# Kernel tuning notes

Measured on AMD Instinct MI355X. Metric: run time of the kernel, lower is better.

## Reference

```python
import jax, jax.numpy as jnp
import numpy as np

DIM = 256      # in_channels == hidden_channels
INNER = 256    # heads * dim_head
HEADS = 4
DH = 64        # dim_head = hidden_channels // num_heads
EDGE_DIM = 512 # 2 * in_channels
FF = 1024      # 4 * dim ff expansion
DEPTH = 2
OUT = 1
N = 50000      # two stacked graphs of 25000 nodes
E = 100000
HALF = 25000


def setup_inputs() -> dict:
    key = jax.random.key(0)
    ks = iter(jax.random.split(key, 32))

    def lin(fan_in, fan_out):
        w = jax.random.normal(next(ks), (DEPTH, fan_in, fan_out), jnp.float32) * (1.0 / np.sqrt(fan_in))
        b = jnp.zeros((DEPTH, fan_out), jnp.float32)
        return w, b

    x = jax.random.normal(next(ks), (N, DIM), jnp.float32)
    edge_index = jax.random.randint(next(ks), (2, E), 0, HALF, dtype=jnp.int32)
    Wq, bq = lin(DIM, INNER)
    Wkv, bkv = lin(DIM, 2 * INNER)
    We, be = lin(EDGE_DIM, INNER)
    Wo, bo = lin(INNER, DIM)
    W1, b1 = lin(DIM, FF)
    W2, b2 = lin(FF, DIM)
    g_attn = jax.random.normal(next(ks), (DEPTH, 3 * DIM, 1), jnp.float32) * (1.0 / np.sqrt(3 * DIM))
    g_ff = jax.random.normal(next(ks), (DEPTH, 3 * DIM, 1), jnp.float32) * (1.0 / np.sqrt(3 * DIM))
    ln1_g = jnp.ones((DEPTH, DIM), jnp.float32); ln1_b = jnp.zeros((DEPTH, DIM), jnp.float32)
    ln2_g = jnp.ones((DEPTH, DIM), jnp.float32); ln2_b = jnp.zeros((DEPTH, DIM), jnp.float32)
    Wout = jax.random.normal(next(ks), (DIM, OUT), jnp.float32) * (1.0 / np.sqrt(DIM))
    bout = jnp.zeros((OUT,), jnp.float32)
    return dict(x=x, edge_index=edge_index, ln1_g=ln1_g, ln1_b=ln1_b, Wq=Wq, bq=bq,
                Wkv=Wkv, bkv=bkv, We=We, be=be, Wo=Wo, bo=bo, g_attn=g_attn,
                ln2_g=ln2_g, ln2_b=ln2_b, W1=W1, b1=b1, W2=W2, b2=b2, g_ff=g_ff,
                Wout=Wout, bout=bout)


def _layer_norm(x, g, b):
    mu = jnp.mean(x, axis=-1, keepdims=True)
    var = jnp.mean(jnp.square(x - mu), axis=-1, keepdims=True)
    return (x - mu) * jax.lax.rsqrt(var + 1e-5) * g + b


def _gated_residual(x, res, w):
    # gate = sigmoid(Linear_no_bias(cat(x, res, x - res)))
    gate = jax.nn.sigmoid(jnp.concatenate([x, res, x - res], axis=-1) @ w)  # [n,1]
    return x * gate + res * (1.0 - gate)


def _forward(x, edge_index, ln1_g, ln1_b, Wq, bq, Wkv, bkv, We, be, Wo, bo, g_attn,
             ln2_g, ln2_b, W1, b1, W2, b2, g_ff, Wout, bout):
    src, dst = edge_index[0], edge_index[1]
    # edge_attr = cat(x[src], x[dst]) as built in DeepGraphTransformer_mse.forward
    edge_attr = jnp.concatenate([x[src], x[dst]], axis=-1)  # [E, 2*DIM]
    nodes = x
    n = nodes.shape[0]
    scale = DH ** -0.5
    for l in range(DEPTH):
        xn = _layer_norm(nodes, ln1_g[l], ln1_b[l])
        q = xn @ Wq[l] + bq[l]                                   # [n, INNER]
        k, v = jnp.split(xn @ Wkv[l] + bkv[l], 2, axis=-1)       # [n, INNER] each
        e = edge_attr @ We[l] + be[l]                            # [E, INNER]
        qe = q[dst].reshape(-1, HEADS, DH)                       # [E,H,Dh]
        ke = (k[src] + e).reshape(-1, HEADS, DH)
        ve = (v[src] + e).reshape(-1, HEADS, DH)
        sim = jnp.einsum('ehd,ehd->eh', qe, ke) * scale          # [E,H]
        smax = jax.ops.segment_max(sim, dst, num_segments=n)     # [n,H] (-inf for empty)
        ez = jnp.exp(sim - smax[dst])
        denom = jax.ops.segment_sum(ez, dst, num_segments=n)
        attn = ez / denom[dst]                                   # softmax over incoming edges
        agg = jax.ops.segment_sum(attn[:, :, None] * ve, dst, num_segments=n)
        attn_out = agg.reshape(n, INNER) @ Wo[l] + bo[l]         # [n, DIM]
        nodes = _gated_residual(attn_out, nodes, g_attn[l])
        xn2 = _layer_norm(nodes, ln2_g[l], ln2_b[l])
        h = jax.nn.gelu(xn2 @ W1[l] + b1[l], approximate=False) @ W2[l] + b2[l]
        nodes = _gated_residual(h, nodes, g_ff[l])
    z = nodes @ Wout + bout                                      # [n, OUT]
    return z


def reference(x, edge_index, ln1_g, ln1_b, Wq, bq, Wkv, bkv, We, be, Wo, bo, g_attn,
              ln2_g, ln2_b, W1, b1, W2, b2, g_ff, Wout, bout):
    z = _forward(x, edge_index, ln1_g, ln1_b, Wq, bq, Wkv, bkv, We, be, Wo, bo, g_attn,
                 ln2_g, ln2_b, W1, b1, W2, b2, g_ff, Wout, bout)
    half = z.shape[0] // 2
    z_old, z_new = z[:half], z[half:]
    return (z_new.reshape(-1), z_old, z_new)
```

## Files before the change

kernel.cpp:

```cpp
#include <hip/hip_runtime.h>
#include <cmath>

#define N_NODES 50000
#define N_EDGES 100000
#define HALF_N  25000
#define DIM     256
#define NDEPTH  2
#define MAXDEG  64

#define WT_QKVE 0
#define WT_WO   393216
#define WT_W1   524288
#define WT_W2   786432
#define WT_LAYER 1048576

typedef __bf16 bf16;
typedef bf16 bf16x8 __attribute__((ext_vector_type(8)));
typedef bf16 bf16x4 __attribute__((ext_vector_type(4)));
typedef float f32x4 __attribute__((ext_vector_type(4)));

__device__ __forceinline__ void lds_barrier() {
  asm volatile("s_waitcnt lgkmcnt(0)" ::: "memory");
  __builtin_amdgcn_s_barrier();
  __builtin_amdgcn_sched_barrier(0);
}

__device__ __forceinline__ float wave_sum(float v) {
  v += __shfl_xor(v, 1);
  v += __shfl_xor(v, 2);
  v += __shfl_xor(v, 4);
  v += __shfl_xor(v, 8);
  v += __shfl_xor(v, 16);
  v += __shfl_xor(v, 32);
  return v;
}

__device__ __forceinline__ float fast_gelu(float x) {
  float p = x * x;
  float q = fmaf(p, -0.10294437f, -2.3022112f);
  float e = exp2f(x * q);
  return x * __builtin_amdgcn_rcpf(1.0f + e);
}

__global__ void ln0_kernel(const float* __restrict__ in, const float* __restrict__ g,
                           const float* __restrict__ b, bf16* __restrict__ A2) {
  int row = blockIdx.x * 4 + (threadIdx.x >> 6);
  if (row >= HALF_N) return;
  int lane = threadIdx.x & 63;
  float4 x = reinterpret_cast<const float4*>(in + (size_t)row * DIM)[lane];
  float mu = wave_sum(x.x + x.y + x.z + x.w) * (1.0f / DIM);
  float d0 = x.x - mu, d1 = x.y - mu, d2 = x.z - mu, d3 = x.w - mu;
  float var = wave_sum(d0*d0 + d1*d1 + d2*d2 + d3*d3) * (1.0f / DIM);
  float r = rsqrtf(var + 1e-5f);
  float4 gv = reinterpret_cast<const float4*>(g)[lane];
  float4 bv = reinterpret_cast<const float4*>(b)[lane];
  bf16x4 o;
  o[0] = (bf16)(d0 * r * gv.x + bv.x);
  o[1] = (bf16)(d1 * r * gv.y + bv.y);
  o[2] = (bf16)(d2 * r * gv.z + bv.z);
  o[3] = (bf16)(d3 * r * gv.w + bv.w);
  *reinterpret_cast<bf16x4*>(A2 + (size_t)row * 512 + lane * 4) = o;
}

template<int KK, int NJ>
__global__ __launch_bounds__(512, 2) void gemm_nloop(
    const bf16* __restrict__ A, const bf16* __restrict__ Wp,
    const float* __restrict__ bias, bf16* __restrict__ C, int M) {
  constexpr int STEPS = KK / 64;
  __shared__ bf16x8 As[KK * 8];
  __shared__ bf16 Cs[64 * 128];
  const int tid = threadIdx.x;
  const int lane = tid & 63, wv = tid >> 6;
  const int lm = lane & 15, kb = (lane >> 4) & 3;
  const int row0 = blockIdx.x * 64;
#pragma unroll
  for (int i = 0; i < KK / 64; ++i) {
    int idx = tid + i * 512;
    int row = idx & 63, k8 = idx >> 6;
    int rga = row0 + row; if (rga >= M) rga = M - 1;
    As[idx] = *reinterpret_cast<const bf16x8*>(A + (size_t)rga * KK + k8 * 8);
  }
  const bf16x8* wb = reinterpret_cast<const bf16x8*>(Wp) + kb * 128 + wv * 16 + lm;
  bf16x8 pfr = wb[0];
  lds_barrier();
  for (int jn = 0; jn < NJ; ++jn) {
    f32x4 acc[4] = {};
#pragma unroll
    for (int st = 0; st < STEPS; ++st) {
#pragma unroll
      for (int ks = 0; ks < 2; ++ks) {
        bf16x8 bfr = (st == 0 && ks == 0)
                   ? pfr
                   : wb[(size_t)jn * (KK * 16) + st * 1024 + ks * 512];
        bf16x8 af[4];
#pragma unroll
        for (int mi = 0; mi < 4; ++mi)
          af[mi] = As[(st * 8 + ks * 4 + kb) * 64 + mi * 16 + lm];
#pragma unroll
        for (int mi = 0; mi < 4; ++mi)
          acc[mi] = __builtin_amdgcn_mfma_f32_16x16x32_bf16(af[mi], bfr, acc[mi], 0, 0, 0);
      }
    }
    if (jn + 1 < NJ) pfr = wb[(size_t)(jn + 1) * (KK * 16)];
    lds_barrier();
    {
      int c = wv * 16 + lm;
      float bval = bias[jn * 128 + c];
#pragma unroll
      for (int mi = 0; mi < 4; ++mi)
#pragma unroll
        for (int e = 0; e < 4; ++e) {
          int r = mi * 16 + kb * 4 + e;
          Cs[r * 128 + c] = (bf16)(acc[mi][e] + bval);
        }
    }
    lds_barrier();
    bf16x8* C8 = reinterpret_cast<bf16x8*>(C);
    const bf16x8* Cs8 = (const bf16x8*)Cs;
#pragma unroll
    for (int i = 0; i < 2; ++i) {
      int idx = tid + i * 512;
      int row = idx >> 4, c8 = idx & 15;
      int grow = row0 + row;
      if (grow < M) C8[(size_t)grow * (NJ * 16) + jn * 16 + c8] = Cs8[row * 16 + c8];
    }
  }
}

__global__ __launch_bounds__(256, 2) void wo_fused(
    const bf16* __restrict__ agg, const bf16* __restrict__ A2,
    const bf16* __restrict__ Wp, const float* __restrict__ bvec,
    const float* __restrict__ bo, const int* __restrict__ deg,
    const float* __restrict__ gattn, const float* __restrict__ ln2g,
    const float* __restrict__ ln2b, float* __restrict__ nodes,
    bf16* __restrict__ xn, int rows) {
  __shared__ bf16x8 As[2048];
  __shared__ bf16 Cs[64 * 256];
  const int tid = threadIdx.x;
  const int lane = tid & 63, wv = tid >> 6;
  const int row0 = blockIdx.x * 64;
  float4 w0 = reinterpret_cast<const float4*>(gattn)[lane];
  float4 w1 = reinterpret_cast<const float4*>(gattn + 256)[lane];
  float4 w2 = reinterpret_cast<const float4*>(gattn + 512)[lane];
  float4 wa, wbv;
  wa.x = w0.x + w2.x; wa.y = w0.y + w2.y; wa.z = w0.z + w2.z; wa.w = w0.w + w2.w;
  wbv.x = w1.x - w2.x; wbv.y = w1.y - w2.y; wbv.z = w1.z - w2.z; wbv.w = w1.w - w2.w;
  float4 gv = reinterpret_cast<const float4*>(ln2g)[lane];
  float4 bv = reinterpret_cast<const float4*>(ln2b)[lane];
  if (row0 < HALF_N) {
    const int wr = wv >> 1, wc = wv & 1;
    const int lm = lane & 15, kb = (lane >> 4) & 3;
#pragma unroll
    for (int i = 0; i < 8; ++i) {
      int idx = tid + i * 256;
      int row = idx & 63, k8 = idx >> 6;
      int rga = row0 + row; if (rga >= HALF_N) rga = HALF_N - 1;
      As[idx] = *reinterpret_cast<const bf16x8*>(agg + (size_t)rga * 256 + k8 * 8);
    }
    bf16x8 afx[2][8];
#pragma unroll
    for (int mi = 0; mi < 2; ++mi) {
      int row = row0 + wr * 32 + mi * 16 + lm;
      if (row >= HALF_N) row = HALF_N - 1;
      const bf16* pa = A2 + (size_t)row * 512 + 256 + kb * 8;
#pragma unroll
      for (int t = 0; t < 8; ++t)
        afx[mi][t] = *reinterpret_cast<const bf16x8*>(pa + t * 32);
    }
    lds_barrier();
    const bf16x8* wb = reinterpret_cast<const bf16x8*>(Wp) + kb * 128 + wc * 64 + lm;
    for (int jn = 0; jn < 2; ++jn) {
      f32x4 acc[2][4] = {};
#pragma unroll
      for (int st = 0; st < 8; ++st) {
#pragma unroll
        for (int ks = 0; ks < 2; ++ks) {
          bf16x8 bfr[4], af[2];
#pragma unroll
          for (int ni = 0; ni < 4; ++ni)
            bfr[ni] = wb[jn * 8192 + (st * 8 + ks * 4) * 128 + ni * 16];
#pragma unroll
          for (int mi = 0; mi < 2; ++mi)
            af[mi] = (st < 4) ? As[(st * 8 + ks * 4 + kb) * 64 + wr * 32 + mi * 16 + lm]
                              : afx[mi][(st - 4) * 2 + ks];
#pragma unroll
          for (int mi = 0; mi < 2; ++mi)
#pragma unroll
            for (int ni = 0; ni < 4; ++ni)
              acc[mi][ni] = __builtin_amdgcn_mfma_f32_16x16x32_bf16(af[mi], bfr[ni], acc[mi][ni], 0, 0, 0);
        }
      }
#pragma unroll
      for (int ni = 0; ni < 4; ++ni) {
        int cfull = jn * 128 + wc * 64 + ni * 16 + lm;
        float bval = bvec[cfull];
#pragma unroll
        for (int mi = 0; mi < 2; ++mi)
#pragma unroll
          for (int e = 0; e < 4; ++e) {
            int r = wr * 32 + mi * 16 + kb * 4 + e;
            int ch = (cfull >> 3) ^ (r & 7);
            Cs[r * 256 + ch * 8 + (cfull & 7)] = (bf16)(acc[mi][ni][e] + bval);
          }
      }
    }
    lds_barrier();
    for (int pass = 0; pass < 16; ++pass) {
      int r = pass * 4 + wv;
      int grow = row0 + r;
      float x0, x1, x2, x3;
      if (grow >= HALF_N || deg[grow] == 0) {
        float4 bo4 = reinterpret_cast<const float4*>(bo)[lane];
        x0 = bo4.x; x1 = bo4.y; x2 = bo4.z; x3 = bo4.w;
      } else {
        int ch = (lane >> 1) ^ (r & 7);
        bf16x4 c4 = *reinterpret_cast<const bf16x4*>(Cs + r * 256 + ch * 8 + (lane & 1) * 4);
        x0 = (float)c4[0]; x1 = (float)c4[1]; x2 = (float)c4[2]; x3 = (float)c4[3];
      }
      float4 rv = reinterpret_cast<const float4*>(nodes + (size_t)grow * 256)[lane];
      float dot = x0 * wa.x + rv.x * wbv.x + x1 * wa.y + rv.y * wbv.y
                + x2 * wa.z + rv.z * wbv.z + x3 * wa.w + rv.w * wbv.w;
      dot = wave_sum(dot);
      float gate = 1.0f / (1.0f + __expf(-dot));
      float n0 = fmaf(x0 - rv.x, gate, rv.x);
      float n1 = fmaf(x1 - rv.y, gate, rv.y);
      float n2 = fmaf(x2 - rv.z, gate, rv.z);
      float n3 = fmaf(x3 - rv.w, gate, rv.w);
      float4 o; o.x = n0; o.y = n1; o.z = n2; o.w = n3;
      reinterpret_cast<float4*>(nodes + (size_t)grow * 256)[lane] = o;
      float mu = wave_sum(n0 + n1 + n2 + n3) * (1.0f / DIM);
      float d0 = n0 - mu, d1 = n1 - mu, d2 = n2 - mu, d3 = n3 - mu;
      float var = wave_sum(d0*d0 + d1*d1 + d2*d2 + d3*d3) * (1.0f / DIM);
      float rs = rsqrtf(var + 1e-5f);
      bf16x4 ob;
      ob[0] = (bf16)(d0 * rs * gv.x + bv.x);
      ob[1] = (bf16)(d1 * rs * gv.y + bv.y);
      ob[2] = (bf16)(d2 * rs * gv.z + bv.z);
      ob[3] = (bf16)(d3 * rs * gv.w + bv.w);
      *reinterpret_cast<bf16x4*>(xn + (size_t)grow * 256 + lane * 4) = ob;
    }
  } else {
    float4 bo4 = reinterpret_cast<const float4*>(bo)[lane];
    for (int pass = 0; pass < 16; ++pass) {
      int grow = row0 + pass * 4 + wv;
      if (grow >= rows) continue;
      float x0 = bo4.x, x1 = bo4.y, x2 = bo4.z, x3 = bo4.w;
      float4 rv = reinterpret_cast<const float4*>(nodes + (size_t)grow * 256)[lane];
      float dot = x0 * wa.x + rv.x * wbv.x + x1 * wa.y + rv.y * wbv.y
                + x2 * wa.z + rv.z * wbv.z + x3 * wa.w + rv.w * wbv.w;
      dot = wave_sum(dot);
      float gate = 1.0f / (1.0f + __expf(-dot));
      float n0 = fmaf(x0 - rv.x, gate, rv.x);
      float n1 = fmaf(x1 - rv.y, gate, rv.y);
      float n2 = fmaf(x2 - rv.z, gate, rv.z);
      float n3 = fmaf(x3 - rv.w, gate, rv.w);
      float4 o; o.x = n0; o.y = n1; o.z = n2; o.w = n3;
      reinterpret_cast<float4*>(nodes + (size_t)grow * 256)[lane] = o;
      float mu = wave_sum(n0 + n1 + n2 + n3) * (1.0f / DIM);
      float d0 = n0 - mu, d1 = n1 - mu, d2 = n2 - mu, d3 = n3 - mu;
      float var = wave_sum(d0*d0 + d1*d1 + d2*d2 + d3*d3) * (1.0f / DIM);
      float rs = rsqrtf(var + 1e-5f);
      bf16x4 ob;
      ob[0] = (bf16)(d0 * rs * gv.x + bv.x);
      ob[1] = (bf16)(d1 * rs * gv.y + bv.y);
      ob[2] = (bf16)(d2 * rs * gv.z + bv.z);
      ob[3] = (bf16)(d3 * rs * gv.w + bv.w);
      *reinterpret_cast<bf16x4*>(xn + (size_t)grow * 256 + lane * 4) = ob;
    }
  }
}

template<int LAST>
__global__ __launch_bounds__(512, 4) void ff_fused(
    const bf16* __restrict__ A, const bf16* __restrict__ W1p,
    const float* __restrict__ b1, const bf16* __restrict__ W2p,
    const float* __restrict__ b2, float* __restrict__ nodes,
    const float* __restrict__ gff, const float* __restrict__ ln1g,
    const float* __restrict__ ln1b, bf16* __restrict__ A2,
    const float* __restrict__ Wout, const float* __restrict__ bout,
    float* __restrict__ out, int M) {
  __shared__ char smem[65536];
  bf16x8* Xs = (bf16x8*)smem;
  bf16*   Cs = (bf16*)smem;
  bf16x8* Hs = (bf16x8*)(smem + 32768);
  const int tid = threadIdx.x;
  const int lane = tid & 63, wv = tid >> 6;
  const int lm = lane & 15, kb = (lane >> 4) & 3;
  const int row0 = blockIdx.x * 64;
#pragma unroll
  for (int i = 0; i < 4; ++i) {
    int idx = tid + i * 512;
    int row = idx & 63, k8 = idx >> 6;
    int rga = row0 + row; if (rga >= M) rga = M - 1;
    Xs[idx] = *reinterpret_cast<const bf16x8*>(A + (size_t)rga * 256 + k8 * 8);
  }
  lds_barrier();
  const bf16x8* w1b = (const bf16x8*)W1p + kb * 128 + wv * 16 + lm;
  const bf16x8* w2b = (const bf16x8*)W2p + kb * 256 + wv * 32 + lm;
  f32x4 acc[4][2] = {};
  for (int j = 0; j < 8; ++j) {
    bf16x8 pf2[4];
#pragma unroll
    for (int ks = 0; ks < 2; ++ks)
#pragma unroll
      for (int ni = 0; ni < 2; ++ni)
        pf2[ks * 2 + ni] = w2b[j * 4096 + ks * 1024 + ni * 16];
    f32x4 acc1[4] = {};
#pragma unroll
    for (int half = 0; half < 2; ++half) {
#pragma unroll
      for (int ks = 0; ks < 4; ++ks) {
        bf16x8 bfr = w1b[j * 4096 + half * 2048 + ks * 512];
        bf16x8 af[4];
#pragma unroll
        for (int mi = 0; mi < 4; ++mi)
          af[mi] = Xs[(half * 16 + ks * 4 + kb) * 64 + mi * 16 + lm];
#pragma unroll
        for (int mi = 0; mi < 4; ++mi)
          acc1[mi] = __builtin_amdgcn_mfma_f32_16x16x32_bf16(af[mi], bfr, acc1[mi], 0, 0, 0);
      }
    }
    {
      bf16* hsb = (bf16*)(Hs + (j & 1) * 1024);
      int c = wv * 16 + lm;
      float bval = b1[j * 128 + c];
#pragma unroll
      for (int mi = 0; mi < 4; ++mi)
#pragma unroll
        for (int e = 0; e < 4; ++e) {
          int r = mi * 16 + kb * 4 + e;
          float v = fast_gelu(acc1[mi][e] + bval);
          hsb[((c >> 3) * 64 + r) * 8 + (c & 7)] = (bf16)v;
        }
    }
    lds_barrier();
    const bf16x8* hb = Hs + (j & 1) * 1024;
#pragma unroll
    for (int h2 = 0; h2 < 2; ++h2) {
#pragma unroll
      for (int ks = 0; ks < 2; ++ks) {
        bf16x8 bfr[2], af[4];
#pragma unroll
        for (int ni = 0; ni < 2; ++ni)
          bfr[ni] = (h2 == 0) ? pf2[ks * 2 + ni]
                              : w2b[j * 4096 + 2048 + ks * 1024 + ni * 16];
#pragma unroll
        for (int mi = 0; mi < 4; ++mi)
          af[mi] = hb[(h2 * 8 + ks * 4 + kb) * 64 + mi * 16 + lm];
#pragma unroll
        for (int mi = 0; mi < 4; ++mi)
#pragma unroll
          for (int ni = 0; ni < 2; ++ni)
            acc[mi][ni] = __builtin_amdgcn_mfma_f32_16x16x32_bf16(af[mi], bfr[ni], acc[mi][ni], 0, 0, 0);
      }
    }
  }
#pragma unroll
  for (int ni = 0; ni < 2; ++ni) {
    int c = wv * 32 + ni * 16 + lm;
    float bval = b2[c];
#pragma unroll
    for (int mi = 0; mi < 4; ++mi)
#pragma unroll
      for (int e = 0; e < 4; ++e) {
        int r = mi * 16 + kb * 4 + e;
        int ch = (c >> 3) ^ (r & 7);
        Cs[r * 256 + ch * 8 + (c & 7)] = (bf16)(acc[mi][ni][e] + bval);
      }
  }
  float4 w0 = reinterpret_cast<const float4*>(gff)[lane];
  float4 w1 = reinterpret_cast<const float4*>(gff + 256)[lane];
  float4 w2 = reinterpret_cast<const float4*>(gff + 512)[lane];
  float4 wa, wbv;
  wa.x = w0.x + w2.x; wa.y = w0.y + w2.y; wa.z = w0.z + w2.z; wa.w = w0.w + w2.w;
  wbv.x = w1.x - w2.x; wbv.y = w1.y - w2.y; wbv.z = w1.z - w2.z; wbv.w = w1.w - w2.w;
  float4 gv, bv, wo4;
  if (LAST) {
    wo4 = reinterpret_cast<const float4*>(Wout)[lane];
  } else {
    gv = reinterpret_cast<const float4*>(ln1g)[lane];
    bv = reinterpret_cast<const float4*>(ln1b)[lane];
  }
  lds_barrier();
  for (int pass = 0; pass < 8; ++pass) {
    int r = pass * 8 + wv;
    int grow = row0 + r;
    if (grow >= M) continue;
    int ch = (lane >> 1) ^ (r & 7);
    bf16x4 c4 = *reinterpret_cast<const bf16x4*>(Cs + r * 256 + ch * 8 + (lane & 1) * 4);
    float x0 = (float)c4[0], x1 = (float)c4[1], x2 = (float)c4[2], x3 = (float)c4[3];
    float4 rv = reinterpret_cast<const float4*>(nodes + (size_t)grow * 256)[lane];
    float dot = x0 * wa.x + rv.x * wbv.x + x1 * wa.y + rv.y * wbv.y
              + x2 * wa.z + rv.z * wbv.z + x3 * wa.w + rv.w * wbv.w;
    dot = wave_sum(dot);
    float gate = 1.0f / (1.0f + __expf(-dot));
    float n0 = fmaf(x0 - rv.x, gate, rv.x);
    float n1 = fmaf(x1 - rv.y, gate, rv.y);
    float n2 = fmaf(x2 - rv.z, gate, rv.z);
    float n3 = fmaf(x3 - rv.w, gate, rv.w);
    if (LAST) {
      float z = n0 * wo4.x + n1 * wo4.y + n2 * wo4.z + n3 * wo4.w;
      z = wave_sum(z);
      if (lane == 0) {
        z += bout[0];
        if (grow < HALF_N) {
          out[HALF_N + grow] = z;
        } else {
          int jj = grow - HALF_N;
          out[jj] = z;
          out[2 * HALF_N + jj] = z;
        }
      }
    } else {
      float4 o; o.x = n0; o.y = n1; o.z = n2; o.w = n3;
      reinterpret_cast<float4*>(nodes + (size_t)grow * 256)[lane] = o;
      if (grow < HALF_N) {
        float mu = wave_sum(n0 + n1 + n2 + n3) * (1.0f / DIM);
        float d0 = n0 - mu, d1 = n1 - mu, d2 = n2 - mu, d3 = n3 - mu;
        float var = wave_sum(d0*d0 + d1*d1 + d2*d2 + d3*d3) * (1.0f / DIM);
        float rs = rsqrtf(var + 1e-5f);
        bf16x4 ob;
        ob[0] = (bf16)(d0 * rs * gv.x + bv.x);
        ob[1] = (bf16)(d1 * rs * gv.y + bv.y);
        ob[2] = (bf16)(d2 * rs * gv.z + bv.z);
        ob[3] = (bf16)(d3 * rs * gv.w + bv.w);
        *reinterpret_cast<bf16x4*>(A2 + (size_t)grow * 512 + lane * 4) = ob;
      }
    }
  }
}

__global__ void ell_build(const int* __restrict__ ei, int* __restrict__ deg,
                          int* __restrict__ ell) {
  int e = blockIdx.x * 256 + threadIdx.x;
  if (e >= N_EDGES) return;
  int s = ei[e], d = ei[N_EDGES + e];
  int pos = atomicAdd(&deg[d], 1);
  if (pos < MAXDEG) ell[d * MAXDEG + pos] = s;
}

__global__ void attn_gather(const int* __restrict__ deg, const int* __restrict__ ell,
                            const bf16* __restrict__ qkv, bf16* __restrict__ agg) {
  int d = blockIdx.x * 4 + (threadIdx.x >> 6);
  if (d >= HALF_N) return;
  int lane = threadIdx.x & 63;
  int cnt = deg[d]; if (cnt > MAXDEG) cnt = MAXDEG;
  const bf16* qr = qkv + (size_t)d * 768;
  bf16x4 qb = *reinterpret_cast<const bf16x4*>(qr + lane * 4);
  float q0 = (float)qb[0], q1 = (float)qb[1], q2 = (float)qb[2], q3 = (float)qb[3];
  float m = -INFINITY, den = 0.0f, a0 = 0.0f, a1 = 0.0f, a2 = 0.0f, a3 = 0.0f;
  int i = 0;
  for (; i + 2 <= cnt; i += 2) {
    int s0 = ell[d * MAXDEG + i];
    int s1 = ell[d * MAXDEG + i + 1];
    bf16x8 k0 = *reinterpret_cast<const bf16x8*>(qkv + (size_t)s0 * 768 + 256 + lane * 8);
    bf16x8 k1 = *reinterpret_cast<const bf16x8*>(qkv + (size_t)s1 * 768 + 256 + lane * 8);
    float p0 = q0 * (float)k0[0] + q1 * (float)k0[1] + q2 * (float)k0[2] + q3 * (float)k0[3];
    float p1 = q0 * (float)k1[0] + q1 * (float)k1[1] + q2 * (float)k1[2] + q3 * (float)k1[3];
    p0 += __shfl_xor(p0, 1); p1 += __shfl_xor(p1, 1);
    p0 += __shfl_xor(p0, 2); p1 += __shfl_xor(p1, 2);
    p0 += __shfl_xor(p0, 4); p1 += __shfl_xor(p1, 4);
    p0 += __shfl_xor(p0, 8); p1 += __shfl_xor(p1, 8);
    float s0v = p0 * 0.125f, s1v = p1 * 0.125f;
    float nm = fmaxf(m, fmaxf(s0v, s1v));
    float sc = __expf(m - nm);
    float w0 = __expf(s0v - nm), w1 = __expf(s1v - nm);
    den = den * sc + w0 + w1;
    a0 = a0 * sc + w0 * (float)k0[4] + w1 * (float)k1[4];
    a1 = a1 * sc + w0 * (float)k0[5] + w1 * (float)k1[5];
    a2 = a2 * sc + w0 * (float)k0[6] + w1 * (float)k1[6];
    a3 = a3 * sc + w0 * (float)k0[7] + w1 * (float)k1[7];
    m = nm;
  }
  if (i < cnt) {
    int s = ell[d * MAXDEG + i];
    bf16x8 kv8 = *reinterpret_cast<const bf16x8*>(qkv + (size_t)s * 768 + 256 + lane * 8);
    float p = q0 * (float)kv8[0] + q1 * (float)kv8[1] + q2 * (float)kv8[2] + q3 * (float)kv8[3];
    p += __shfl_xor(p, 1); p += __shfl_xor(p, 2);
    p += __shfl_xor(p, 4); p += __shfl_xor(p, 8);
    float sim = p * 0.125f;
    float nm = fmaxf(m, sim);
    float sc = __expf(m - nm);
    float w = __expf(sim - nm);
    den = den * sc + w;
    a0 = a0 * sc + w * (float)kv8[4];
    a1 = a1 * sc + w * (float)kv8[5];
    a2 = a2 * sc + w * (float)kv8[6];
    a3 = a3 * sc + w * (float)kv8[7];
    m = nm;
  }
  bf16x4 o;
  if (cnt > 0) {
    float inv = 1.0f / den;
    o[0] = (bf16)(a0 * inv);
    o[1] = (bf16)(a1 * inv);
    o[2] = (bf16)(a2 * inv);
    o[3] = (bf16)(a3 * inv);
  } else {
    o[0] = (bf16)0.0f; o[1] = (bf16)0.0f; o[2] = (bf16)0.0f; o[3] = (bf16)0.0f;
  }
  *reinterpret_cast<bf16x4*>(agg + (size_t)d * DIM + lane * 4) = o;
}

__global__ void prep_w(const float* __restrict__ Wq, const float* __restrict__ Wkv,
                       const float* __restrict__ We, const float* __restrict__ Wo,
                       const float* __restrict__ W1, const float* __restrict__ W2,
                       bf16* __restrict__ wt) {
  int idx = blockIdx.x * 256 + threadIdx.x;
  if (idx >= 2 * WT_LAYER) return;
  int l = idx / WT_LAYER, r = idx % WT_LAYER;
  float v;
  if (r < 393216) {
    int jn = r >> 16, t = r & 65535;
    int k8 = t >> 10, u = t & 1023, n = u >> 3, e = u & 7;
    int ncol = jn * 128 + n, k = k8 * 8 + e;
    if (ncol < 256) {
      v = (k < 256) ? Wq[l * 65536 + k * 256 + ncol] : 0.0f;
    } else {
      int u2 = ncol - 256;
      int c = (u2 >> 3) * 4 + (u2 & 3);
      int half = (u2 >> 2) & 1;
      if (k < 256) v = Wkv[l * 131072 + k * 512 + half * 256 + c];
      else         v = We[l * 131072 + (k - 256) * 256 + c];
    }
  } else if (r < 524288) {
    int rr = r - 393216;
    int jn = rr >> 16, t = rr & 65535;
    int k8 = t >> 10, u = t & 1023, n = u >> 3, e = u & 7;
    int k = k8 * 8 + e;
    if (k >= 256) return;
    v = Wo[l * 65536 + k * 256 + jn * 128 + n];
  } else if (r < 786432) {
    int rr = r - 524288;
    int j = rr >> 15, t = rr & 32767;
    int k8 = t >> 10, u = t & 1023, n = u >> 3, e = u & 7;
    v = W1[l * 262144 + (k8 * 8 + e) * 1024 + j * 128 + n];
  } else {
    int rr = r - 786432;
    int j = rr >> 15, t = rr & 32767;
    int k8 = t >> 11, u = t & 2047, n = u >> 3, e = u & 7;
    v = W2[l * 262144 + (j * 128 + k8 * 8 + e) * 256 + n];
  }
  wt[idx] = (bf16)v;
}

__global__ void prep_weff(const float* __restrict__ We, const float* __restrict__ Wo,
                          bf16* __restrict__ wt) {
  int idx = blockIdx.x * 256 + threadIdx.x;
  if (idx >= 2 * 65536) return;
  int l = idx >> 16, r = idx & 65535;
  int k = r >> 8, n = r & 255;
  const float* wer = We + l * 131072 + (256 + k) * 256;
  const float* wor = Wo + l * 65536 + n;
  float acc = 0.0f;
#pragma unroll 4
  for (int m = 0; m < 256; ++m) acc += wer[m] * wor[m * 256];
  int kf = 256 + k;
  size_t off = (size_t)l * WT_LAYER + WT_WO +
               (n >> 7) * 65536 + (kf >> 3) * 1024 + (n & 127) * 8 + (kf & 7);
  wt[off] = (bf16)acc;
}

__global__ void prep_bvec(const float* __restrict__ be, const float* __restrict__ Wo,
                          const float* __restrict__ bo, float* __restrict__ biasq) {
  int idx = blockIdx.x * 256 + threadIdx.x;
  if (idx >= 512) return;
  int l = idx >> 8, n = idx & 255;
  const float* ber = be + l * 256;
  const float* wor = Wo + l * 65536 + n;
  float acc = bo[l * 256 + n];
#pragma unroll 4
  for (int m = 0; m < 256; ++m) acc += ber[m] * wor[m * 256];
  biasq[1536 + l * 256 + n] = acc;
}

__global__ void prep_bias(const float* __restrict__ bq, const float* __restrict__ bkv,
                          float* __restrict__ biasq) {
  int i = blockIdx.x * 256 + threadIdx.x;
  if (i >= 1536) return;
  int l = i / 768, n = i % 768;
  float v;
  if (n < 256) v = bq[l * 256 + n];
  else {
    int u2 = n - 256;
    int c = (u2 >> 3) * 4 + (u2 & 3);
    int half = (u2 >> 2) & 1;
    v = bkv[l * 512 + half * 256 + c];
  }
  biasq[i] = v;
}

__global__ void prep_x(const float* __restrict__ x, bf16* __restrict__ A2) {
  int i = blockIdx.x * 256 + threadIdx.x;
  if (i >= HALF_N * 64) return;
  int row = i >> 6, c = i & 63;
  float4 v = reinterpret_cast<const float4*>(x)[i];
  bf16x4 o;
  o[0] = (bf16)v.x; o[1] = (bf16)v.y; o[2] = (bf16)v.z; o[3] = (bf16)v.w;
  *reinterpret_cast<bf16x4*>(A2 + (size_t)row * 512 + 256 + c * 4) = o;
}

extern "C" void kernel_launch(void* const* d_in, const int* in_sizes, int n_in,
                              void* d_out, int out_size, void* d_ws, size_t ws_size,
                              hipStream_t stream) {
  const float* x     = (const float*)d_in[0];
  const int*   ei    = (const int*)d_in[1];
  const float* ln1_g = (const float*)d_in[2];
  const float* ln1_b = (const float*)d_in[3];
  const float* Wq    = (const float*)d_in[4];
  const float* bq    = (const float*)d_in[5];
  const float* Wkv   = (const float*)d_in[6];
  const float* bkv   = (const float*)d_in[7];
  const float* We    = (const float*)d_in[8];
  const float* be    = (const float*)d_in[9];
  const float* Wo    = (const float*)d_in[10];
  const float* bo    = (const float*)d_in[11];
  const float* g_attn= (const float*)d_in[12];
  const float* ln2_g = (const float*)d_in[13];
  const float* ln2_b = (const float*)d_in[14];
  const float* W1    = (const float*)d_in[15];
  const float* b1    = (const float*)d_in[16];
  const float* W2    = (const float*)d_in[17];
  const float* b2    = (const float*)d_in[18];
  const float* g_ff  = (const float*)d_in[19];
  const float* Wout  = (const float*)d_in[20];
  const float* bout  = (const float*)d_in[21];
  float* out = (float*)d_out;

  char* base = (char*)d_ws;
  float* nodes   = (float*)base;  base += (size_t)N_NODES * DIM * 4;
  bf16*  A2      = (bf16*)base;   base += (size_t)HALF_N * 512 * 2;
  bf16*  xn_bf   = (bf16*)base;   base += (size_t)N_NODES * DIM * 2;
  bf16*  qkv     = (bf16*)base;   base += (size_t)HALF_N * 768 * 2;
  bf16*  agg     = (bf16*)base;   base += (size_t)HALF_N * DIM * 2;
  bf16*  wt      = (bf16*)base;   base += (size_t)2 * WT_LAYER * 2;
  float* biasq   = (float*)base;  base += 2048 * 4;
  int*   deg     = (int*)base;    base += HALF_N * 4;
  int*   ell     = (int*)base;    base += (size_t)HALF_N * MAXDEG * 4;

  hipMemcpyAsync(nodes, x, (size_t)N_NODES * DIM * sizeof(float),
                 hipMemcpyDeviceToDevice, stream);
  prep_w<<<(2 * WT_LAYER + 255) / 256, 256, 0, stream>>>(Wq, Wkv, We, Wo, W1, W2, wt);
  prep_weff<<<(2 * 65536 + 255) / 256, 256, 0, stream>>>(We, Wo, wt);
  prep_bvec<<<2, 256, 0, stream>>>(be, Wo, bo, biasq);
  prep_bias<<<6, 256, 0, stream>>>(bq, bkv, biasq);
  prep_x<<<(HALF_N * 64 + 255) / 256, 256, 0, stream>>>(x, A2);
  hipMemsetAsync(deg, 0, HALF_N * sizeof(int), stream);
  ell_build<<<(N_EDGES + 255) / 256, 256, 0, stream>>>(ei, deg, ell);

  const int GP_H = (HALF_N + 63) / 64;
  const int GP_N = (N_NODES + 63) / 64;

  for (int l = 0; l < NDEPTH; ++l) {
    const bf16* wl = wt + (size_t)l * WT_LAYER;
    if (l == 0)
      ln0_kernel<<<(HALF_N + 3) / 4, 256, 0, stream>>>(x, ln1_g, ln1_b, A2);
    gemm_nloop<512, 6><<<GP_H, 512, 0, stream>>>(A2, wl + WT_QKVE, biasq + l * 768, qkv, HALF_N);
    attn_gather<<<(HALF_N + 3) / 4, 256, 0, stream>>>(deg, ell, qkv, agg);
    wo_fused<<<GP_N, 256, 0, stream>>>(agg, A2, wl + WT_WO, biasq + 1536 + l * 256,
                                       bo + l * DIM, deg, g_attn + l * 768,
                                       ln2_g + l * DIM, ln2_b + l * DIM,
                                       nodes, xn_bf, N_NODES);
    if (l < NDEPTH - 1) {
      ff_fused<0><<<GP_N, 512, 0, stream>>>(
          xn_bf, wl + WT_W1, b1 + l * 1024, wl + WT_W2, b2 + l * DIM,
          nodes, g_ff + l * 768, ln1_g + (l + 1) * DIM, ln1_b + (l + 1) * DIM, A2,
          nullptr, nullptr, nullptr, N_NODES);
    } else {
      ff_fused<1><<<GP_N, 512, 0, stream>>>(
          xn_bf, wl + WT_W1, b1 + l * 1024, wl + WT_W2, b2 + l * DIM,
          nodes, g_ff + l * 768, nullptr, nullptr, nullptr,
          Wout, bout, out, N_NODES);
    }
  }
}
```

Before: 468.2 us.

## Retile fused FF kernel warps into 2x4 grid with transposed first GEMM

Result: slower. 525.8 us (+12.3%).

```diff
diff --git a/kernel.cpp b/kernel.cpp
--- a/kernel.cpp
+++ b/kernel.cpp
@@ -285,6 +285,7 @@
   bf16x8* Hs = (bf16x8*)(smem + 32768);
   const int tid = threadIdx.x;
   const int lane = tid & 63, wv = tid >> 6;
+  const int wr = wv >> 2, wc = wv & 3;
   const int lm = lane & 15, kb = (lane >> 4) & 3;
   const int row0 = blockIdx.x * 64;
 #pragma unroll
@@ -295,43 +296,53 @@
     Xs[idx] = *reinterpret_cast<const bf16x8*>(A + (size_t)rga * 256 + k8 * 8);
   }
   lds_barrier();
-  const bf16x8* w1b = (const bf16x8*)W1p + kb * 128 + wv * 16 + lm;
-  const bf16x8* w2b = (const bf16x8*)W2p + kb * 256 + wv * 32 + lm;
-  f32x4 acc[4][2] = {};
+  const bf16x8* w1p8 = (const bf16x8*)W1p;
+  const bf16x8* w2p8 = (const bf16x8*)W2p;
+  f32x4 acc[2][4] = {};
   for (int j = 0; j < 8; ++j) {
     bf16x8 pf2[4];
 #pragma unroll
     for (int ks = 0; ks < 2; ++ks)
 #pragma unroll
       for (int ni = 0; ni < 2; ++ni)
-        pf2[ks * 2 + ni] = w2b[j * 4096 + ks * 1024 + ni * 16];
-    f32x4 acc1[4] = {};
+        pf2[ks * 2 + ni] = w2p8[j * 4096 + (ks * 4 + kb) * 256 + wc * 64 + ni * 16 + lm];
+    f32x4 acc1[2][2] = {};
 #pragma unroll
     for (int half = 0; half < 2; ++half) {
 #pragma unroll
       for (int ks = 0; ks < 4; ++ks) {
-        bf16x8 bfr = w1b[j * 4096 + half * 2048 + ks * 512];
-        bf16x8 af[4];
-#pragma unroll
-        for (int mi = 0; mi < 4; ++mi)
-          af[mi] = Xs[(half * 16 + ks * 4 + kb) * 64 + mi * 16 + lm];
-#pragma unroll
-        for (int mi = 0; mi < 4; ++mi)
-          acc1[mi] = __builtin_amdgcn_mfma_f32_16x16x32_bf16(af[mi], bfr, acc1[mi], 0, 0, 0);
+        int k8i = half * 16 + ks * 4 + kb;
+        bf16x8 wf[2], af[2];
+#pragma unroll
+        for (int ni = 0; ni < 2; ++ni)
+          wf[ni] = w1p8[j * 4096 + k8i * 128 + wc * 32 + ni * 16 + lm];
+#pragma unroll
+        for (int mi = 0; mi < 2; ++mi)
+          af[mi] = Xs[k8i * 64 + wr * 32 + mi * 16 + lm];
+#pragma unroll
+        for (int mi = 0; mi < 2; ++mi)
+#pragma unroll
+          for (int ni = 0; ni < 2; ++ni)
+            acc1[mi][ni] = __builtin_amdgcn_mfma_f32_16x16x32_bf16(wf[ni], af[mi], acc1[mi][ni], 0, 0, 0);
       }
     }
     {
       bf16* hsb = (bf16*)(Hs + (j & 1) * 1024);
-      int c = wv * 16 + lm;
-      float bval = b1[j * 128 + c];
-#pragma unroll
-      for (int mi = 0; mi < 4; ++mi)
-#pragma unroll
-        for (int e = 0; e < 4; ++e) {
-          int r = mi * 16 + kb * 4 + e;
-          float v = fast_gelu(acc1[mi][e] + bval);
-          hsb[((c >> 3) * 64 + r) * 8 + (c & 7)] = (bf16)v;
+#pragma unroll
+      for (int ni = 0; ni < 2; ++ni) {
+        float4 bb = *reinterpret_cast<const float4*>(b1 + j * 128 + wc * 32 + ni * 16 + kb * 4);
+        int k8o = wc * 4 + ni * 2 + (kb >> 1);
+#pragma unroll
+        for (int mi = 0; mi < 2; ++mi) {
+          int xr = wr * 32 + mi * 16 + lm;
+          bf16x4 hv;
+          hv[0] = (bf16)fast_gelu(acc1[mi][ni][0] + bb.x);
+          hv[1] = (bf16)fast_gelu(acc1[mi][ni][1] + bb.y);
+          hv[2] = (bf16)fast_gelu(acc1[mi][ni][2] + bb.z);
+          hv[3] = (bf16)fast_gelu(acc1[mi][ni][3] + bb.w);
+          *reinterpret_cast<bf16x4*>(hsb + (k8o * 64 + xr) * 8 + (kb & 1) * 4) = hv;
         }
+      }
     }
     lds_barrier();
     const bf16x8* hb = Hs + (j & 1) * 1024;
@@ -339,31 +350,32 @@
     for (int h2 = 0; h2 < 2; ++h2) {
 #pragma unroll
       for (int ks = 0; ks < 2; ++ks) {
-        bf16x8 bfr[2], af[4];
-#pragma unroll
-        for (int ni = 0; ni < 2; ++ni)
-          bfr[ni] = (h2 == 0) ? pf2[ks * 2 + ni]
-                              : w2b[j * 4096 + 2048 + ks * 1024 + ni * 16];
-#pragma unroll
-        for (int mi = 0; mi < 4; ++mi)
-          af[mi] = hb[(h2 * 8 + ks * 4 + kb) * 64 + mi * 16 + lm];
-#pragma unroll
-        for (int mi = 0; mi < 4; ++mi)
-#pragma unroll
-          for (int ni = 0; ni < 2; ++ni)
+        bf16x8 bfr[4], af[2];
+#pragma unroll
+        for (int ni = 0; ni < 4; ++ni)
+          bfr[ni] = (h2 == 0 && ni < 2)
+                  ? pf2[ks * 2 + ni]
+                  : w2p8[j * 4096 + (h2 * 8 + ks * 4 + kb) * 256 + wc * 64 + ni * 16 + lm];
+#pragma unroll
+        for (int mi = 0; mi < 2; ++mi)
+          af[mi] = hb[(h2 * 8 + ks * 4 + kb) * 64 + wr * 32 + mi * 16 + lm];
+#pragma unroll
+        for (int mi = 0; mi < 2; ++mi)
+#pragma unroll
+          for (int ni = 0; ni < 4; ++ni)
             acc[mi][ni] = __builtin_amdgcn_mfma_f32_16x16x32_bf16(af[mi], bfr[ni], acc[mi][ni], 0, 0, 0);
       }
     }
   }
 #pragma unroll
-  for (int ni = 0; ni < 2; ++ni) {
-    int c = wv * 32 + ni * 16 + lm;
+  for (int ni = 0; ni < 4; ++ni) {
+    int c = wc * 64 + ni * 16 + lm;
     float bval = b2[c];
 #pragma unroll
-    for (int mi = 0; mi < 4; ++mi)
+    for (int mi = 0; mi < 2; ++mi)
 #pragma unroll
       for (int e = 0; e < 4; ++e) {
-        int r = mi * 16 + kb * 4 + e;
+        int r = wr * 32 + mi * 16 + kb * 4 + e;
         int ch = (c >> 3) ^ (r & 7);
         Cs[r * 256 + ch * 8 + (c & 7)] = (bf16)(acc[mi][ni][e] + bval);
       }
```
